# Performance work log

Hardware: AMD Instinct MI355X
Metric: run time of the kernel (lower is better)

The kernel has to match this reference:

```python
import jax, jax.numpy as jnp
import numpy as np

HEADS = 16
D_MODEL = 1024
MAX_LEN = 1024
BATCH = 4
SEQ = 1024


def _skew(QEr):
    # Transformer-XL / Music-Transformer skew trick.
    # QEr: [B, H, L, L] -> pad one zero column on the left, reshape, drop first row.
    B, H, L, _ = QEr.shape
    padded = jnp.pad(QEr, ((0, 0), (0, 0), (0, 0), (1, 0)))  # [B,H,L,L+1]
    reshaped = padded.reshape(B, H, L + 1, L)
    return reshaped[:, :, 1:, :]  # [B,H,L,L]


def setup_inputs() -> dict:
    key = jax.random.key(0)
    ks = jax.random.split(key, 8)
    d = D_MODEL // HEADS
    std = 0.05  # tf.random_normal_initializer default stddev
    return {
        "query": jax.random.normal(ks[0], (BATCH, SEQ, D_MODEL), jnp.float32),
        "key": jax.random.normal(ks[1], (BATCH, SEQ, D_MODEL), jnp.float32),
        "value": jax.random.normal(ks[2], (BATCH, SEQ, D_MODEL), jnp.float32),
        "WQ": std * jax.random.normal(ks[3], (D_MODEL, D_MODEL), jnp.float32),
        "WK": std * jax.random.normal(ks[4], (D_MODEL, D_MODEL), jnp.float32),
        "WV": std * jax.random.normal(ks[5], (D_MODEL, D_MODEL), jnp.float32),
        "Er": std * jax.random.normal(ks[6], (MAX_LEN, d), jnp.float32),
        "WMerge": std * jax.random.normal(ks[7], (D_MODEL, D_MODEL), jnp.float32),
    }


def reference(query, key, value, WQ, WK, WV, Er, WMerge):
    B, L, D = query.shape
    H = HEADS
    d = D // H
    # Faithful to source: plain reshape (NOT transpose-based head split).
    q = (query @ WQ).reshape(B, H, L, d)          # [B,H,L,d]
    k_t = (key @ WK).reshape(B, H, d, L)          # [B,H,d,L]
    v = (value @ WV).reshape(B, H, L, d)          # [B,H,L,d]
    start = MAX_LEN - L
    Er_t = Er[start:, :].T                        # [d, L]
    QEr = q @ Er_t                                # [B,H,L,L]
    Srel = _skew(QEr)                             # [B,H,L,L]
    attn = (q @ k_t + Srel) / jnp.sqrt(jnp.asarray(d, q.dtype))
    attn = jax.nn.softmax(attn, axis=-1)
    out = attn @ v                                # [B,H,L,d]
    out = out.transpose(0, 2, 1, 3).reshape(B, L, D)
    return out @ WMerge
```

## Files before the change

### kernel.cpp

```cpp
#include <hip/hip_runtime.h>

#define H_  16
#define L_  1024
#define D_  1024
#define DH  64

typedef short bf16x8 __attribute__((ext_vector_type(8)));
typedef float f32x4  __attribute__((ext_vector_type(4)));

__device__ __forceinline__ ushort f2bf(float f) {
  union { float f; unsigned int u; } x; x.f = f;
  unsigned int u = x.u;
  u = (u + 0x7fffu + ((u >> 16) & 1u)) >> 16;
  return (ushort)u;
}
__device__ __forceinline__ float bf2f(ushort s) {
  union { unsigned int u; float f; } x; x.u = ((unsigned int)s) << 16;
  return x.f;
}

__device__ __forceinline__ unsigned int pkbf(float a, float b) {
  union { float f; unsigned int u; } xa, xb; xa.f = a; xb.f = b;
  unsigned int ua = xa.u + 0x8000u;
  unsigned int ub = xb.u + 0x8000u;
  return (ua >> 16) | (ub & 0xffff0000u);
}
__device__ __forceinline__ ushort lo16(unsigned int v) { return (ushort)v; }
__device__ __forceinline__ ushort hi16(unsigned int v) { return (ushort)(v >> 16); }

__device__ __forceinline__ size_t afi(int m, int k) {
  return (((size_t)((m >> 7) * 32 + (k >> 5)) * 8 + ((m >> 4) & 7)) << 9)
       + ((size_t)((((k >> 3) & 3) << 4) + (m & 15)) << 3) + (k & 7);
}

__device__ __forceinline__ void gl_lds16(const ushort* g, ushort* l) {
  __builtin_amdgcn_global_load_lds(
      (const __attribute__((address_space(1))) void*)g,
      (__attribute__((address_space(3))) void*)l, 16, 0, 0);
}

__global__ __launch_bounds__(256) void cvt3_kernel(
    const float* __restrict__ q, const float* __restrict__ k, const float* __restrict__ v,
    ushort* __restrict__ qb, ushort* __restrict__ kb, ushort* __restrict__ vb) {
  const int z = blockIdx.y;
  const float* in = (z == 0) ? q : (z == 1) ? k : v;
  ushort* out = (z == 0) ? qb : (z == 1) ? kb : vb;
  int idx = (blockIdx.x * 256 + threadIdx.x) * 8;
  int m = idx >> 10, kk = idx & 1023;
  float4 f0 = *(const float4*)(in + idx);
  float4 f1 = *(const float4*)(in + idx + 4);
  uint4 o;
  o.x = pkbf(f0.x, f0.y); o.y = pkbf(f0.z, f0.w);
  o.z = pkbf(f1.x, f1.y); o.w = pkbf(f1.z, f1.w);
  *(uint4*)(out + afi(m, kk)) = o;
}

__global__ __launch_bounds__(256) void erF_kernel(const float* __restrict__ Er,
                                                  ushort* __restrict__ ErF) {
  int t = blockIdx.x * 256 + threadIdx.x;
  int lane = t & 63, ph = (t >> 6) & 1, jg = t >> 7;
  int m = jg * 16 + (lane & 15);
  int k = ph * 32 + (lane >> 4) * 8;
  float4 f0 = *(const float4*)(Er + m * 64 + k);
  float4 f1 = *(const float4*)(Er + m * 64 + k + 4);
  uint4 o;
  o.x = pkbf(f0.x, f0.y); o.y = pkbf(f0.z, f0.w);
  o.z = pkbf(f1.x, f1.y); o.w = pkbf(f1.z, f1.w);
  *(uint4*)(ErF + t * 8) = o;
}

__global__ __launch_bounds__(256) void wT4_kernel(
    const float* __restrict__ W0, const float* __restrict__ W1,
    const float* __restrict__ W2, const float* __restrict__ W3,
    ushort* __restrict__ T0, ushort* __restrict__ T1,
    ushort* __restrict__ T2, ushort* __restrict__ T3) {
  __shared__ ushort tt[64][72];
  const int z = blockIdx.z;
  const float* W = (z == 0) ? W0 : (z == 1) ? W1 : (z == 2) ? W2 : W3;
  ushort*     WT = (z == 0) ? T0 : (z == 1) ? T1 : (z == 2) ? T2 : T3;
  const int t = threadIdx.x;
  const int k0 = blockIdx.y * 64, n0 = blockIdx.x * 64;
#pragma unroll
  for (int c = 0; c < 4; ++c) {
    int k = c * 16 + (t >> 4);
    float4 f = *(const float4*)(W + (size_t)(k0 + k) * 1024 + n0 + (t & 15) * 4);
    unsigned int p01 = pkbf(f.x, f.y), p23 = pkbf(f.z, f.w);
    tt[(t & 15) * 4 + 0][k] = lo16(p01);
    tt[(t & 15) * 4 + 1][k] = hi16(p01);
    tt[(t & 15) * 4 + 2][k] = lo16(p23);
    tt[(t & 15) * 4 + 3][k] = hi16(p23);
  }
  __syncthreads();
#pragma unroll
  for (int p = 0; p < 2; ++p) {
    int n = p * 32 + (t >> 3);
    *(uint4*)(WT + afi(n0 + n, k0 + (t & 7) * 8)) = *(const uint4*)(&tt[n][(t & 7) * 8]);
  }
}

__global__ __launch_bounds__(256) void gemm_qkv_kernel(
    const ushort* __restrict__ Aq, const ushort* __restrict__ Ak, const ushort* __restrict__ Av,
    const ushort* __restrict__ BTq, const ushort* __restrict__ BTk, const ushort* __restrict__ BTv,
    ushort* __restrict__ Cq, ushort* __restrict__ Ck, ushort* __restrict__ Cv) {
  __shared__ ushort lsA[4096];
  __shared__ ushort lsB[4096];
  const int z = blockIdx.z;
  const ushort* A  = (z == 0) ? Aq  : (z == 1) ? Ak  : Av;
  const ushort* BT = (z == 0) ? BTq : (z == 1) ? BTk : BTv;
  ushort*       Cp = (z == 0) ? Cq  : (z == 1) ? Ck  : Cv;

  const int tid  = threadIdx.x;
  const int w    = tid >> 6, lane = tid & 63, qd = lane >> 4, ln = lane & 15;
  const int rw   = w >> 1, cw = w & 1;
  const int mb   = blockIdx.y, nb = blockIdx.x;
  const int m0   = mb * 128, n0 = nb * 128;

  f32x4 acc[16];
#pragma unroll
  for (int i = 0; i < 16; ++i) acc[i] = (f32x4){0.f, 0.f, 0.f, 0.f};

  for (int kb = 0; kb < 32; ++kb) {
    const ushort* Ab = A  + ((size_t)(mb * 32 + kb) << 12);
    const ushort* Bb = BT + ((size_t)(nb * 32 + kb) << 12);
    const int c0 = 2 * w;
    gl_lds16(Ab + ((size_t)c0 << 9) + lane * 8,        lsA + (c0 << 9));
    gl_lds16(Ab + ((size_t)(c0 + 1) << 9) + lane * 8,  lsA + ((c0 + 1) << 9));
    gl_lds16(Bb + ((size_t)c0 << 9) + lane * 8,        lsB + (c0 << 9));
    gl_lds16(Bb + ((size_t)(c0 + 1) << 9) + lane * 8,  lsB + ((c0 + 1) << 9));
    __syncthreads();
    bf16x8 afr[4], bfr[4];
#pragma unroll
    for (int am = 0; am < 4; ++am)
      afr[am] = *(const bf16x8*)(lsA + ((rw * 4 + am) << 9) + lane * 8);
#pragma unroll
    for (int bn = 0; bn < 4; ++bn)
      bfr[bn] = *(const bf16x8*)(lsB + ((cw * 4 + bn) << 9) + lane * 8);
#pragma unroll
    for (int am = 0; am < 4; ++am)
#pragma unroll
      for (int bn = 0; bn < 4; ++bn)
        acc[am * 4 + bn] = __builtin_amdgcn_mfma_f32_16x16x32_bf16(afr[am], bfr[bn], acc[am * 4 + bn], 0, 0, 0);
    __syncthreads();
  }
#pragma unroll
  for (int am = 0; am < 4; ++am)
#pragma unroll
    for (int bn = 0; bn < 4; ++bn) {
      const int rbase = m0 + rw * 64 + am * 16 + qd * 4;
      const int colg  = n0 + cw * 64 + bn * 16 + ln;
      const unsigned int p01 = pkbf(acc[am * 4 + bn][0], acc[am * 4 + bn][1]);
      const unsigned int p23 = pkbf(acc[am * 4 + bn][2], acc[am * 4 + bn][3]);
      if (z == 0) {
        Cp[(size_t)(rbase + 0) * 1024 + colg] = lo16(p01);
        Cp[(size_t)(rbase + 1) * 1024 + colg] = hi16(p01);
        Cp[(size_t)(rbase + 2) * 1024 + colg] = lo16(p23);
        Cp[(size_t)(rbase + 3) * 1024 + colg] = hi16(p23);
      } else if (z == 1) {
        const int bh  = rbase >> 6;
        const int ki0 = rbase & 63;
        const int jg  = colg >> 4;
        const int ph  = ki0 >> 5;
        const int lanep = ((ki0 >> 3) & 3) * 16 + (colg & 15);
        const int jj0 = ki0 & 7;
        uint2 uu; uu.x = p01; uu.y = p23;
        *(uint2*)(Cp + (size_t)bh * 65536 + (size_t)((jg * 2 + ph) * 64 + lanep) * 8 + jj0) = uu;
      } else {
        const int bh = rbase >> 6;
        const int llow = colg >> 6, dd = colg & 63;
        const int g = dd >> 4, lnf = dd & 15;
        const ushort vals[4] = {lo16(p01), hi16(p01), lo16(p23), hi16(p23)};
#pragma unroll
        for (int r = 0; r < 4; ++r) {
          int l = ((rbase + r) & 63) * 16 + llow;
          int ks = l >> 5;
          int lanep = ((l >> 3) & 3) * 16 + lnf;
          int jj = l & 7;
          Cp[(size_t)bh * 65536 + (size_t)((g * 32 + ks) * 64 + lanep) * 8 + jj] = vals[r];
        }
      }
    }
}

__global__ __launch_bounds__(512) void gemm_mg_kernel(const ushort* __restrict__ A,
                                                      const ushort* __restrict__ BT,
                                                      float* __restrict__ Cp) {
  __shared__ ushort lsA[2][4096];
  __shared__ ushort lsB[2][4096];
  __shared__ float  mgred[256 * 33];
  const int tid  = threadIdx.x;
  const int w    = tid >> 6, lane = tid & 63, qd = lane >> 4, ln = lane & 15;
  const int kh   = w >> 2, q = w & 3;
  const int rw   = q >> 1, cw = q & 1;
  const int mb   = blockIdx.y, nb = blockIdx.x;
  const int m0   = mb * 128, n0 = nb * 128;

  f32x4 acc[16];
#pragma unroll
  for (int i = 0; i < 16; ++i) acc[i] = (f32x4){0.f, 0.f, 0.f, 0.f};

  for (int kb = 0; kb < 16; ++kb) {
    const int kbi = kh * 16 + kb;
    const ushort* Ab = A  + ((size_t)(mb * 32 + kbi) << 12);
    const ushort* Bb = BT + ((size_t)(nb * 32 + kbi) << 12);
    const int c0 = 2 * q;
    gl_lds16(Ab + ((size_t)c0 << 9) + lane * 8,        lsA[kh] + (c0 << 9));
    gl_lds16(Ab + ((size_t)(c0 + 1) << 9) + lane * 8,  lsA[kh] + ((c0 + 1) << 9));
    gl_lds16(Bb + ((size_t)c0 << 9) + lane * 8,        lsB[kh] + (c0 << 9));
    gl_lds16(Bb + ((size_t)(c0 + 1) << 9) + lane * 8,  lsB[kh] + ((c0 + 1) << 9));
    __syncthreads();
    bf16x8 afr[4], bfr[4];
#pragma unroll
    for (int am = 0; am < 4; ++am)
      afr[am] = *(const bf16x8*)(lsA[kh] + ((rw * 4 + am) << 9) + lane * 8);
#pragma unroll
    for (int bn = 0; bn < 4; ++bn)
      bfr[bn] = *(const bf16x8*)(lsB[kh] + ((cw * 4 + bn) << 9) + lane * 8);
#pragma unroll
    for (int am = 0; am < 4; ++am)
#pragma unroll
      for (int bn = 0; bn < 4; ++bn)
        acc[am * 4 + bn] = __builtin_amdgcn_mfma_f32_16x16x32_bf16(afr[am], bfr[bn], acc[am * 4 + bn], 0, 0, 0);
    __syncthreads();
  }

  for (int half = 0; half < 2; ++half) {
    __syncthreads();
    if (w >= 4) {
      const int base = ((w - 4) * 64 + lane) * 33;
#pragma unroll
      for (int i = 0; i < 8; ++i)
#pragma unroll
        for (int c = 0; c < 4; ++c) mgred[base + i * 4 + c] = acc[half * 8 + i][c];
    }
    __syncthreads();
    if (w < 4) {
      const int base = (w * 64 + lane) * 33;
#pragma unroll
      for (int i = 0; i < 8; ++i)
#pragma unroll
        for (int c = 0; c < 4; ++c) acc[half * 8 + i][c] += mgred[base + i * 4 + c];
    }
  }
  if (w < 4) {
#pragma unroll
    for (int am = 0; am < 4; ++am)
#pragma unroll
      for (int bn = 0; bn < 4; ++bn) {
        const int rbase = m0 + rw * 64 + am * 16 + qd * 4;
        const int colg  = n0 + cw * 64 + bn * 16 + ln;
#pragma unroll
        for (int r = 0; r < 4; ++r)
          Cp[(size_t)(rbase + r) * 1024 + colg] = acc[am * 4 + bn][r];
      }
  }
}

__global__ __launch_bounds__(512, 4) void attn_kernel(
    const ushort* __restrict__ QW, const ushort* __restrict__ KF,
    const ushort* __restrict__ VF, const ushort* __restrict__ ErF,
    ushort* __restrict__ Om) {
  __shared__ ushort qflat[17440];
  __shared__ float  red[4][64][4];
  __shared__ float  stats[2][8][16];

  const int tid  = threadIdx.x;
  const int w    = tid >> 6;
  const int lane = tid & 63;
  const int qd   = lane >> 4;
  const int ln   = lane & 15;
  const int bh   = blockIdx.y;
  const int i0   = blockIdx.x << 4;
  const ushort* q  = QW + ((size_t)bh << 16);
  const ushort* kf = KF + ((size_t)bh << 16);
  const ushort* vf = VF + ((size_t)bh << 16);

  if (tid < 16) qflat[tid * 1025 + 1024] = 0;

  bf16x8 a00 = *(const bf16x8*)(q + (size_t)(i0 + ln) * 64 + qd * 8);
  bf16x8 a01 = *(const bf16x8*)(q + (size_t)(i0 + ln) * 64 + 32 + qd * 8);
  const int row16 = (i0 + 16 > 1023) ? 1023 : i0 + 16;
  bf16x8 a10 = *(const bf16x8*)(q + (size_t)row16 * 64 + qd * 8);
  bf16x8 a11 = *(const bf16x8*)(q + (size_t)row16 * 64 + 32 + qd * 8);

  const int jg0 = w * 8;

#pragma unroll
  for (int f = 0; f < 8; ++f) {
    const int jg = jg0 + f;
    bf16x8 b0 = *(const bf16x8*)(ErF + (size_t)((jg * 2 + 0) * 64 + lane) * 8);
    bf16x8 b1 = *(const bf16x8*)(ErF + (size_t)((jg * 2 + 1) * 64 + lane) * 8);
    f32x4 acc = {0.f, 0.f, 0.f, 0.f};
    acc = __builtin_amdgcn_mfma_f32_16x16x32_bf16(a00, b0, acc, 0, 0, 0);
    acc = __builtin_amdgcn_mfma_f32_16x16x32_bf16(a01, b1, acc, 0, 0, 0);
    const int m = jg * 16 + ln;
    const unsigned int p01 = pkbf(acc[0], acc[1]);
    const unsigned int p23 = pkbf(acc[2], acc[3]);
    qflat[(qd * 4 + 0) * 1025 + m] = lo16(p01);
    qflat[(qd * 4 + 1) * 1025 + m] = hi16(p01);
    qflat[(qd * 4 + 2) * 1025 + m] = lo16(p23);
    qflat[(qd * 4 + 3) * 1025 + m] = hi16(p23);
    if (jg * 16 <= 1006 - i0) {
      f32x4 ac2 = {0.f, 0.f, 0.f, 0.f};
      ac2 = __builtin_amdgcn_mfma_f32_16x16x32_bf16(a10, b0, ac2, 0, 0, 0);
      ac2 = __builtin_amdgcn_mfma_f32_16x16x32_bf16(a11, b1, ac2, 0, 0, 0);
      if (qd == 0) qflat[16 * 1025 + m] = f2bf(ac2[0]);
    }
  }

  f32x4 sfr[8];
#pragma unroll
  for (int f = 0; f < 8; ++f) {
    const int jg = jg0 + f;
    bf16x8 b0 = *(const bf16x8*)(kf + (size_t)((jg * 2 + 0) * 64 + lane) * 8);
    bf16x8 b1 = *(const bf16x8*)(kf + (size_t)((jg * 2 + 1) * 64 + lane) * 8);
    f32x4 acc = {0.f, 0.f, 0.f, 0.f};
    acc = __builtin_amdgcn_mfma_f32_16x16x32_bf16(a00, b0, acc, 0, 0, 0);
    acc = __builtin_amdgcn_mfma_f32_16x16x32_bf16(a01, b1, acc, 0, 0, 0);
    sfr[f] = acc;
  }
  __syncthreads();

#pragma unroll
  for (int f = 0; f < 8; ++f) {
    const int cj = 1023 - i0 + w * 128 + f * 16 + ln;
#pragma unroll
    for (int r = 0; r < 4; ++r)
      sfr[f][r] += bf2f(qflat[(qd * 4 + r) * 1024 + cj]);
  }

  {
    float vm[4];
#pragma unroll
    for (int r = 0; r < 4; ++r) {
      float m = sfr[0][r];
#pragma unroll
      for (int f = 1; f < 8; ++f) m = fmaxf(m, sfr[f][r]);
#pragma unroll
      for (int off = 1; off < 16; off <<= 1) m = fmaxf(m, __shfl_xor(m, off, 64));
      vm[r] = m;
    }
    if (ln == 0) {
#pragma unroll
      for (int r = 0; r < 4; ++r) stats[0][w][qd * 4 + r] = vm[r];
    }
  }
  __syncthreads();
  const float cexp = 0.18033688011112042f;
  float gm2[4];
#pragma unroll
  for (int r = 0; r < 4; ++r) {
    float m = stats[0][0][qd * 4 + r];
#pragma unroll
    for (int ww = 1; ww < 8; ++ww) m = fmaxf(m, stats[0][ww][qd * 4 + r]);
    gm2[r] = -m * cexp;
  }

  float vs[4] = {0.f, 0.f, 0.f, 0.f};
#pragma unroll
  for (int f = 0; f < 8; ++f) {
    const int j = w * 128 + f * 16 + ln;
    const float e0 = exp2f(fmaf(sfr[f][0], cexp, gm2[0]));
    const float e1 = exp2f(fmaf(sfr[f][1], cexp, gm2[1]));
    const float e2 = exp2f(fmaf(sfr[f][2], cexp, gm2[2]));
    const float e3 = exp2f(fmaf(sfr[f][3], cexp, gm2[3]));
    vs[0] += e0; vs[1] += e1; vs[2] += e2; vs[3] += e3;
    const unsigned int p01 = pkbf(e0, e1);
    const unsigned int p23 = pkbf(e2, e3);
    qflat[(qd * 4 + 0) * 1048 + j] = lo16(p01);
    qflat[(qd * 4 + 1) * 1048 + j] = hi16(p01);
    qflat[(qd * 4 + 2) * 1048 + j] = lo16(p23);
    qflat[(qd * 4 + 3) * 1048 + j] = hi16(p23);
  }
#pragma unroll
  for (int r = 0; r < 4; ++r) {
    float s = vs[r];
#pragma unroll
    for (int off = 1; off < 16; off <<= 1) s += __shfl_xor(s, off, 64);
    if (ln == 0) stats[1][w][qd * 4 + r] = s;
  }
  __syncthreads();
  float rrl[4];
#pragma unroll
  for (int r = 0; r < 4; ++r) {
    float s = 0.f;
#pragma unroll
    for (int ww = 0; ww < 8; ++ww) s += stats[1][ww][qd * 4 + r];
    rrl[r] = 1.0f / s;
  }

  const int g = w & 3, kh = w >> 2;
  f32x4 oacc0 = {0.f, 0.f, 0.f, 0.f};
  f32x4 oacc1 = {0.f, 0.f, 0.f, 0.f};
#pragma unroll
  for (int kc = 0; kc < 16; kc += 2) {
    const int ks0 = kh * 16 + kc;
    const int ks1 = ks0 + 1;
    bf16x8 ap0 = *(const bf16x8*)(qflat + ln * 1048 + ks0 * 32 + qd * 8);
    bf16x8 bv0 = *(const bf16x8*)(vf + (size_t)((g * 32 + ks0) * 64 + lane) * 8);
    oacc0 = __builtin_amdgcn_mfma_f32_16x16x32_bf16(ap0, bv0, oacc0, 0, 0, 0);
    bf16x8 ap1 = *(const bf16x8*)(qflat + ln * 1048 + ks1 * 32 + qd * 8);
    bf16x8 bv1 = *(const bf16x8*)(vf + (size_t)((g * 32 + ks1) * 64 + lane) * 8);
    oacc1 = __builtin_amdgcn_mfma_f32_16x16x32_bf16(ap1, bv1, oacc1, 0, 0, 0);
  }
  f32x4 oacc = oacc0 + oacc1;

  if (w >= 4) {
#pragma unroll
    for (int cc = 0; cc < 4; ++cc) red[w - 4][lane][cc] = oacc[cc];
  }
  __syncthreads();
  if (w < 4) {
    const int b = bh >> 4, h = bh & 15;
    const int kg = h * 64 + g * 16 + ln;
    const int mbase = b * 1024 + i0;
    ushort* ob = Om + (((size_t)((mbase >> 7) * 32 + (kg >> 5)) * 8 + ((mbase >> 4) & 7)) << 9)
               + ((((kg >> 3) & 3) * 16 + qd * 4) << 3) + (kg & 7);
    const float o0 = (oacc[0] + red[w][lane][0]) * rrl[0];
    const float o1 = (oacc[1] + red[w][lane][1]) * rrl[1];
    const float o2 = (oacc[2] + red[w][lane][2]) * rrl[2];
    const float o3 = (oacc[3] + red[w][lane][3]) * rrl[3];
    const unsigned int p01 = pkbf(o0, o1);
    const unsigned int p23 = pkbf(o2, o3);
    ob[0]  = lo16(p01);
    ob[8]  = hi16(p01);
    ob[16] = lo16(p23);
    ob[24] = hi16(p23);
  }
}

extern "C" void kernel_launch(void* const* d_in, const int* in_sizes, int n_in,
                              void* d_out, int out_size, void* d_ws, size_t ws_size,
                              hipStream_t stream) {
  const float* query = (const float*)d_in[0];
  const float* key   = (const float*)d_in[1];
  const float* value = (const float*)d_in[2];
  const float* WQ    = (const float*)d_in[3];
  const float* WK    = (const float*)d_in[4];
  const float* WV    = (const float*)d_in[5];
  const float* Er    = (const float*)d_in[6];
  const float* WM    = (const float*)d_in[7];
  float* out = (float*)d_out;

  ushort* QW  = (ushort*)d_ws;
  ushort* KF  = QW  + (size_t)4096 * 1024;
  ushort* VF  = KF  + (size_t)4096 * 1024;
  ushort* O   = VF  + (size_t)4096 * 1024;
  ushort* ErF = O   + (size_t)4096 * 1024;
  ushort* WTQ = ErF + (size_t)65536;
  ushort* WTK = WTQ + (size_t)1024 * 1024;
  ushort* WTV = WTK + (size_t)1024 * 1024;
  ushort* WTM = WTV + (size_t)1024 * 1024;
  ushort* KB  = WTM + (size_t)1024 * 1024;
  ushort* VB  = KB  + (size_t)4096 * 1024;
  ushort* QB  = O;

  cvt3_kernel<<<dim3(2048, 3), 256, 0, stream>>>(query, key, value, QB, KB, VB);
  wT4_kernel<<<dim3(16, 16, 4), 256, 0, stream>>>(WQ, WK, WV, WM, WTQ, WTK, WTV, WTM);
  erF_kernel<<<32, 256, 0, stream>>>(Er, ErF);

  gemm_qkv_kernel<<<dim3(8, 32, 3), 256, 0, stream>>>(QB, KB, VB,
                                                      WTQ, WTK, WTV,
                                                      QW, KF, VF);

  attn_kernel<<<dim3(64, 64), 512, 0, stream>>>(QW, KF, VF, ErF, O);

  gemm_mg_kernel<<<dim3(8, 32), 512, 0, stream>>>(O, WTM, out);
}
```

Measured before the change: 273.3 us.

## Process 32 query rows per attention block and drop cross-wave PV reduction

Each attention block now handles 32 query rows instead of 16, so every Er and K fragment loaded from global memory feeds two MFMA row tiles, and the grid is halved. The PV stage splits waves by row half instead of key half, which removes the shared-memory partial-sum buffer and its extra barrier. A bank-swizzle function is added to the skew buffer indexing. The cost is doubled LDS use (about 68KB) and register pressure, which may cut occupancy under launch_bounds(512,4).

After: 280.2 us. 1.03x slower.

```diff
diff --git a/kernel.cpp b/kernel.cpp
--- a/kernel.cpp
+++ b/kernel.cpp
@@ -27,6 +27,8 @@
 }
 __device__ __forceinline__ ushort lo16(unsigned int v) { return (ushort)v; }
 __device__ __forceinline__ ushort hi16(unsigned int v) { return (ushort)(v >> 16); }
+
+__device__ __forceinline__ int SZ(int F) { return F ^ (((F >> 12) & 3) << 4); }
 
 __device__ __forceinline__ size_t afi(int m, int k) {
   return (((size_t)((m >> 7) * 32 + (k >> 5)) * 8 + ((m >> 4) & 7)) << 9)
@@ -259,9 +261,8 @@
     const ushort* __restrict__ QW, const ushort* __restrict__ KF,
     const ushort* __restrict__ VF, const ushort* __restrict__ ErF,
     ushort* __restrict__ Om) {
-  __shared__ ushort qflat[17440];
-  __shared__ float  red[4][64][4];
-  __shared__ float  stats[2][8][16];
+  __shared__ ushort qflat[33856];
+  __shared__ float  stats[2][8][32];
 
   const int tid  = threadIdx.x;
   const int w    = tid >> 6;
@@ -269,18 +270,20 @@
   const int qd   = lane >> 4;
   const int ln   = lane & 15;
   const int bh   = blockIdx.y;
-  const int i0   = blockIdx.x << 4;
+  const int i0   = blockIdx.x << 5;
   const ushort* q  = QW + ((size_t)bh << 16);
   const ushort* kf = KF + ((size_t)bh << 16);
   const ushort* vf = VF + ((size_t)bh << 16);
 
-  if (tid < 16) qflat[tid * 1025 + 1024] = 0;
+  if (tid < 33) qflat[SZ(tid * 1025 + 1024)] = 0;
 
   bf16x8 a00 = *(const bf16x8*)(q + (size_t)(i0 + ln) * 64 + qd * 8);
   bf16x8 a01 = *(const bf16x8*)(q + (size_t)(i0 + ln) * 64 + 32 + qd * 8);
-  const int row16 = (i0 + 16 > 1023) ? 1023 : i0 + 16;
-  bf16x8 a10 = *(const bf16x8*)(q + (size_t)row16 * 64 + qd * 8);
-  bf16x8 a11 = *(const bf16x8*)(q + (size_t)row16 * 64 + 32 + qd * 8);
+  bf16x8 a10 = *(const bf16x8*)(q + (size_t)(i0 + 16 + ln) * 64 + qd * 8);
+  bf16x8 a11 = *(const bf16x8*)(q + (size_t)(i0 + 16 + ln) * 64 + 32 + qd * 8);
+  const int row32 = (i0 + 32 > 1023) ? 1023 : i0 + 32;
+  bf16x8 a20 = *(const bf16x8*)(q + (size_t)row32 * 64 + qd * 8);
+  bf16x8 a21 = *(const bf16x8*)(q + (size_t)row32 * 64 + 32 + qd * 8);
 
   const int jg0 = w * 8;
 
@@ -289,25 +292,27 @@
     const int jg = jg0 + f;
     bf16x8 b0 = *(const bf16x8*)(ErF + (size_t)((jg * 2 + 0) * 64 + lane) * 8);
     bf16x8 b1 = *(const bf16x8*)(ErF + (size_t)((jg * 2 + 1) * 64 + lane) * 8);
-    f32x4 acc = {0.f, 0.f, 0.f, 0.f};
-    acc = __builtin_amdgcn_mfma_f32_16x16x32_bf16(a00, b0, acc, 0, 0, 0);
-    acc = __builtin_amdgcn_mfma_f32_16x16x32_bf16(a01, b1, acc, 0, 0, 0);
+    f32x4 acc0 = {0.f, 0.f, 0.f, 0.f};
+    acc0 = __builtin_amdgcn_mfma_f32_16x16x32_bf16(a00, b0, acc0, 0, 0, 0);
+    acc0 = __builtin_amdgcn_mfma_f32_16x16x32_bf16(a01, b1, acc0, 0, 0, 0);
+    f32x4 acc1 = {0.f, 0.f, 0.f, 0.f};
+    acc1 = __builtin_amdgcn_mfma_f32_16x16x32_bf16(a10, b0, acc1, 0, 0, 0);
+    acc1 = __builtin_amdgcn_mfma_f32_16x16x32_bf16(a11, b1, acc1, 0, 0, 0);
     const int m = jg * 16 + ln;
-    const unsigned int p01 = pkbf(acc[0], acc[1]);
-    const unsigned int p23 = pkbf(acc[2], acc[3]);
-    qflat[(qd * 4 + 0) * 1025 + m] = lo16(p01);
-    qflat[(qd * 4 + 1) * 1025 + m] = hi16(p01);
-    qflat[(qd * 4 + 2) * 1025 + m] = lo16(p23);
-    qflat[(qd * 4 + 3) * 1025 + m] = hi16(p23);
-    if (jg * 16 <= 1006 - i0) {
+#pragma unroll
+    for (int r = 0; r < 4; ++r) {
+      qflat[SZ((qd * 4 + r) * 1025 + m)]        = f2bf(acc0[r]);
+      qflat[SZ((16 + qd * 4 + r) * 1025 + m)]   = f2bf(acc1[r]);
+    }
+    if (jg * 16 <= 990 - i0) {
       f32x4 ac2 = {0.f, 0.f, 0.f, 0.f};
-      ac2 = __builtin_amdgcn_mfma_f32_16x16x32_bf16(a10, b0, ac2, 0, 0, 0);
-      ac2 = __builtin_amdgcn_mfma_f32_16x16x32_bf16(a11, b1, ac2, 0, 0, 0);
-      if (qd == 0) qflat[16 * 1025 + m] = f2bf(ac2[0]);
-    }
-  }
-
-  f32x4 sfr[8];
+      ac2 = __builtin_amdgcn_mfma_f32_16x16x32_bf16(a20, b0, ac2, 0, 0, 0);
+      ac2 = __builtin_amdgcn_mfma_f32_16x16x32_bf16(a21, b1, ac2, 0, 0, 0);
+      if (qd == 0) qflat[SZ(32 * 1025 + m)] = f2bf(ac2[0]);
+    }
+  }
+
+  f32x4 sfr0[8], sfr1[8];
 #pragma unroll
   for (int f = 0; f < 8; ++f) {
     const int jg = jg0 + f;
@@ -316,7 +321,11 @@
     f32x4 acc = {0.f, 0.f, 0.f, 0.f};
     acc = __builtin_amdgcn_mfma_f32_16x16x32_bf16(a00, b0, acc, 0, 0, 0);
     acc = __builtin_amdgcn_mfma_f32_16x16x32_bf16(a01, b1, acc, 0, 0, 0);
-    sfr[f] = acc;
+    sfr0[f] = acc;
+    f32x4 ac1 = {0.f, 0.f, 0.f, 0.f};
+    ac1 = __builtin_amdgcn_mfma_f32_16x16x32_bf16(a10, b0, ac1, 0, 0, 0);
+    ac1 = __builtin_amdgcn_mfma_f32_16x16x32_bf16(a11, b1, ac1, 0, 0, 0);
+    sfr1[f] = ac1;
   }
   __syncthreads();
 
@@ -324,101 +333,109 @@
   for (int f = 0; f < 8; ++f) {
     const int cj = 1023 - i0 + w * 128 + f * 16 + ln;
 #pragma unroll
-    for (int r = 0; r < 4; ++r)
-      sfr[f][r] += bf2f(qflat[(qd * 4 + r) * 1024 + cj]);
+    for (int r = 0; r < 4; ++r) {
+      sfr0[f][r] += bf2f(qflat[SZ((qd * 4 + r) * 1024 + cj)]);
+      sfr1[f][r] += bf2f(qflat[SZ((16 + qd * 4 + r) * 1024 + cj)]);
+    }
   }
 
   {
-    float vm[4];
+    float vm0[4], vm1[4];
 #pragma unroll
     for (int r = 0; r < 4; ++r) {
-      float m = sfr[0][r];
-#pragma unroll
-      for (int f = 1; f < 8; ++f) m = fmaxf(m, sfr[f][r]);
-#pragma unroll
-      for (int off = 1; off < 16; off <<= 1) m = fmaxf(m, __shfl_xor(m, off, 64));
-      vm[r] = m;
+      float m0 = sfr0[0][r], m1 = sfr1[0][r];
+#pragma unroll
+      for (int f = 1; f < 8; ++f) { m0 = fmaxf(m0, sfr0[f][r]); m1 = fmaxf(m1, sfr1[f][r]); }
+#pragma unroll
+      for (int off = 1; off < 16; off <<= 1) {
+        m0 = fmaxf(m0, __shfl_xor(m0, off, 64));
+        m1 = fmaxf(m1, __shfl_xor(m1, off, 64));
+      }
+      vm0[r] = m0; vm1[r] = m1;
     }
     if (ln == 0) {
 #pragma unroll
-      for (int r = 0; r < 4; ++r) stats[0][w][qd * 4 + r] = vm[r];
+      for (int r = 0; r < 4; ++r) {
+        stats[0][w][qd * 4 + r]      = vm0[r];
+        stats[0][w][16 + qd * 4 + r] = vm1[r];
+      }
     }
   }
   __syncthreads();
   const float cexp = 0.18033688011112042f;
-  float gm2[4];
+  float gm20[4], gm21[4];
 #pragma unroll
   for (int r = 0; r < 4; ++r) {
-    float m = stats[0][0][qd * 4 + r];
-#pragma unroll
-    for (int ww = 1; ww < 8; ++ww) m = fmaxf(m, stats[0][ww][qd * 4 + r]);
-    gm2[r] = -m * cexp;
-  }
-
-  float vs[4] = {0.f, 0.f, 0.f, 0.f};
+    float m0 = stats[0][0][qd * 4 + r], m1 = stats[0][0][16 + qd * 4 + r];
+#pragma unroll
+    for (int ww = 1; ww < 8; ++ww) {
+      m0 = fmaxf(m0, stats[0][ww][qd * 4 + r]);
+      m1 = fmaxf(m1, stats[0][ww][16 + qd * 4 + r]);
+    }
+    gm20[r] = -m0 * cexp; gm21[r] = -m1 * cexp;
+  }
+
+  float vs0[4] = {0.f, 0.f, 0.f, 0.f};
+  float vs1[4] = {0.f, 0.f, 0.f, 0.f};
 #pragma unroll
   for (int f = 0; f < 8; ++f) {
     const int j = w * 128 + f * 16 + ln;
-    const float e0 = exp2f(fmaf(sfr[f][0], cexp, gm2[0]));
-    const float e1 = exp2f(fmaf(sfr[f][1], cexp, gm2[1]));
-    const float e2 = exp2f(fmaf(sfr[f][2], cexp, gm2[2]));
-    const float e3 = exp2f(fmaf(sfr[f][3], cexp, gm2[3]));
-    vs[0] += e0; vs[1] += e1; vs[2] += e2; vs[3] += e3;
-    const unsigned int p01 = pkbf(e0, e1);
-    const unsigned int p23 = pkbf(e2, e3);
-    qflat[(qd * 4 + 0) * 1048 + j] = lo16(p01);
-    qflat[(qd * 4 + 1) * 1048 + j] = hi16(p01);
-    qflat[(qd * 4 + 2) * 1048 + j] = lo16(p23);
-    qflat[(qd * 4 + 3) * 1048 + j] = hi16(p23);
+#pragma unroll
+    for (int r = 0; r < 4; ++r) {
+      const float e0 = exp2f(fmaf(sfr0[f][r], cexp, gm20[r]));
+      const float e1 = exp2f(fmaf(sfr1[f][r], cexp, gm21[r]));
+      vs0[r] += e0; vs1[r] += e1;
+      qflat[(qd * 4 + r) * 1048 + j]        = f2bf(e0);
+      qflat[(16 + qd * 4 + r) * 1048 + j]   = f2bf(e1);
+    }
   }
 #pragma unroll
   for (int r = 0; r < 4; ++r) {
-    float s = vs[r];
-#pragma unroll
-    for (int off = 1; off < 16; off <<= 1) s += __shfl_xor(s, off, 64);
-    if (ln == 0) stats[1][w][qd * 4 + r] = s;
+    float s0 = vs0[r], s1 = vs1[r];
+#pragma unroll
+    for (int off = 1; off < 16; off <<= 1) {
+      s0 += __shfl_xor(s0, off, 64);
+      s1 += __shfl_xor(s1, off, 64);
+    }
+    if (ln == 0) { stats[1][w][qd * 4 + r] = s0; stats[1][w][16 + qd * 4 + r] = s1; }
   }
   __syncthreads();
-  float rrl[4];
+  float rrl0[4], rrl1[4];
 #pragma unroll
   for (int r = 0; r < 4; ++r) {
-    float s = 0.f;
-#pragma unroll
-    for (int ww = 0; ww < 8; ++ww) s += stats[1][ww][qd * 4 + r];
-    rrl[r] = 1.0f / s;
-  }
-
-  const int g = w & 3, kh = w >> 2;
+    float s0 = 0.f, s1 = 0.f;
+#pragma unroll
+    for (int ww = 0; ww < 8; ++ww) {
+      s0 += stats[1][ww][qd * 4 + r];
+      s1 += stats[1][ww][16 + qd * 4 + r];
+    }
+    rrl0[r] = 1.0f / s0; rrl1[r] = 1.0f / s1;
+  }
+
+  const int g = w & 3, rh = w >> 2;
   f32x4 oacc0 = {0.f, 0.f, 0.f, 0.f};
   f32x4 oacc1 = {0.f, 0.f, 0.f, 0.f};
 #pragma unroll
-  for (int kc = 0; kc < 16; kc += 2) {
-    const int ks0 = kh * 16 + kc;
-    const int ks1 = ks0 + 1;
-    bf16x8 ap0 = *(const bf16x8*)(qflat + ln * 1048 + ks0 * 32 + qd * 8);
-    bf16x8 bv0 = *(const bf16x8*)(vf + (size_t)((g * 32 + ks0) * 64 + lane) * 8);
+  for (int ks = 0; ks < 32; ks += 2) {
+    bf16x8 ap0 = *(const bf16x8*)(qflat + (rh * 16 + ln) * 1048 + ks * 32 + qd * 8);
+    bf16x8 bv0 = *(const bf16x8*)(vf + (size_t)((g * 32 + ks) * 64 + lane) * 8);
     oacc0 = __builtin_amdgcn_mfma_f32_16x16x32_bf16(ap0, bv0, oacc0, 0, 0, 0);
-    bf16x8 ap1 = *(const bf16x8*)(qflat + ln * 1048 + ks1 * 32 + qd * 8);
-    bf16x8 bv1 = *(const bf16x8*)(vf + (size_t)((g * 32 + ks1) * 64 + lane) * 8);
+    bf16x8 ap1 = *(const bf16x8*)(qflat + (rh * 16 + ln) * 1048 + (ks + 1) * 32 + qd * 8);
+    bf16x8 bv1 = *(const bf16x8*)(vf + (size_t)((g * 32 + ks + 1) * 64 + lane) * 8);
     oacc1 = __builtin_amdgcn_mfma_f32_16x16x32_bf16(ap1, bv1, oacc1, 0, 0, 0);
   }
   f32x4 oacc = oacc0 + oacc1;
 
-  if (w >= 4) {
-#pragma unroll
-    for (int cc = 0; cc < 4; ++cc) red[w - 4][lane][cc] = oacc[cc];
-  }
-  __syncthreads();
-  if (w < 4) {
+  {
     const int b = bh >> 4, h = bh & 15;
     const int kg = h * 64 + g * 16 + ln;
-    const int mbase = b * 1024 + i0;
+    const int mbase = b * 1024 + i0 + rh * 16;
     ushort* ob = Om + (((size_t)((mbase >> 7) * 32 + (kg >> 5)) * 8 + ((mbase >> 4) & 7)) << 9)
                + ((((kg >> 3) & 3) * 16 + qd * 4) << 3) + (kg & 7);
-    const float o0 = (oacc[0] + red[w][lane][0]) * rrl[0];
-    const float o1 = (oacc[1] + red[w][lane][1]) * rrl[1];
-    const float o2 = (oacc[2] + red[w][lane][2]) * rrl[2];
-    const float o3 = (oacc[3] + red[w][lane][3]) * rrl[3];
+    const float o0 = oacc[0] * (rh ? rrl1[0] : rrl0[0]);
+    const float o1 = oacc[1] * (rh ? rrl1[1] : rrl0[1]);
+    const float o2 = oacc[2] * (rh ? rrl1[2] : rrl0[2]);
+    const float o3 = oacc[3] * (rh ? rrl1[3] : rrl0[3]);
     const unsigned int p01 = pkbf(o0, o1);
     const unsigned int p23 = pkbf(o2, o3);
     ob[0]  = lo16(p01);
@@ -462,7 +479,7 @@
                                                       WTQ, WTK, WTV,
                                                       QW, KF, VF);
 
-  attn_kernel<<<dim3(64, 64), 512, 0, stream>>>(QW, KF, VF, ErF, O);
+  attn_kernel<<<dim3(32, 64), 512, 0, stream>>>(QW, KF, VF, ErF, O);
 
   gemm_mg_kernel<<<dim3(8, 32), 512, 0, stream>>>(O, WTM, out);
 }
```
